# Kernel tuning notes

Hardware: AMD Instinct MI355X
Metric: run time of the kernel (lower is better)

Reference implementation:

```python
import jax, jax.numpy as jnp
import numpy as np
import math

NP2 = 64      # number of RF pulses
V = 32768     # number of voxels


def _shift_matrix(kmax):
    """EPG shift matrix, exact translation of EPG_shift_matrices."""
    N = 3 * (kmax + 1)
    S = np.zeros(N * N, dtype=np.complex64)
    kidx = list(range(3, N, 3)); sidx = [x - 3 for x in kidx]
    S[[a + N * b for a, b in zip(kidx, sidx)]] = 1
    kidx = list(range(4, N, 3)); kidx.pop(); sidx = [x + 3 for x in kidx]
    S[[a + N * b for a, b in zip(kidx, sidx)]] = 1
    kidx = list(range(2, N, 3))
    S[[a + N * b for a, b in zip(kidx, kidx)]] = 1
    S = S.reshape(N, N).T.copy()
    S[0:2, 4] = 1
    return jnp.asarray(S, dtype=jnp.complex64)


def _rf_rot_all(theta):
    """RF rotation matrices for all pulses at once. theta: [P] complex -> [P,3,3]."""
    a = jnp.abs(theta)
    phi = jnp.angle(theta)
    ca2 = (jnp.cos(a / 2) ** 2).astype(jnp.complex64)
    sa2 = jnp.sin(a / 2) ** 2
    sa = jnp.sin(a)
    ca = jnp.cos(a).astype(jnp.complex64)
    ep = jnp.exp(1j * phi)
    em = jnp.exp(-1j * phi)
    e2m = jnp.exp(-2j * phi)
    r00 = ca2
    r10 = e2m * sa2
    r20 = -0.5j * em * sa
    r01 = jnp.conj(r10)
    r11 = ca2
    r21 = 0.5j * ep * sa
    r02 = -1j * ep * sa
    r12 = 1j * em * sa
    r22 = ca
    row0 = jnp.stack([r00, r01, r02], axis=-1)
    row1 = jnp.stack([r10, r11, r12], axis=-1)
    row2 = jnp.stack([r20, r21, r22], axis=-1)
    return jnp.stack([row0, row1, row2], axis=-2).astype(jnp.complex64)


def _epg_gre_f0(theta, T1, T2, TR):
    """Single-compartment GRE EPG recurrence. Returns F0 signal [V, np2].

    Uses full-width (kmax) state updates every pulse: states beyond
    kmax_per_pulse are exactly zero on the ramp-up and cannot influence
    F0 on the ramp-down, so F0 matches the variable-width torch loop.
    """
    np2 = theta.shape[0]
    kmax = np2 - 1
    kpp_max = math.ceil(np2 / 2)
    if kpp_max < kmax:
        kmax = kpp_max
    K = kmax + 1
    N = 3 * K
    v = T1.shape[0]

    St = _shift_matrix(kmax).T                      # [N,N], so S @ f == f @ St
    E1 = jnp.exp(-TR / T1)[:, 0]                    # [V]
    E2 = jnp.exp(-TR / T2)[:, 0]                    # [V]
    # diagonal of kron(I_K, diag(E2,E2,E1)) per voxel -> [V,N]
    e = jnp.tile(jnp.stack([E2, E2, E1], axis=1), (1, K)).astype(jnp.complex64)
    b = jnp.zeros((v, N), jnp.complex64).at[:, 2].set((1 - E1).astype(jnp.complex64))

    A_all = _rf_rot_all(theta)                      # [np2,3,3]
    FF0 = jnp.zeros((v, N), jnp.complex64).at[:, 2].set(1.0)

    def step(FF, A):
        # block-diag kron(I_K, A) applied to the state vector
        Fcol = jnp.einsum('ab,vkb->vka', A, FF.reshape(v, K, 3)).reshape(v, N)
        # relaxation * shift + recovery
        FFn = e * (Fcol @ St) + b
        FFn = FFn.at[:, 0].set(jnp.conj(FFn[:, 0]))
        return FFn, Fcol[:, 0]

    _, F0 = jax.lax.scan(step, FF0, A_all)          # F0: [np2, V]
    return F0.T                                     # [V, np2]


def setup_inputs() -> dict:
    key = jax.random.key(0)
    k1, k2, k3, k4, k5 = jax.random.split(key, 5)
    flip = jax.random.uniform(k1, (NP2,), minval=0.1, maxval=math.pi / 2)
    phase = jax.random.uniform(k2, (NP2,), minval=-math.pi, maxval=math.pi)
    theta_re = (flip * jnp.cos(phase)).astype(jnp.float32)
    theta_im = (flip * jnp.sin(phase)).astype(jnp.float32)
    PD = jax.random.uniform(k3, (V, 1), minval=0.2, maxval=1.0)
    T1 = jax.random.uniform(k4, (V, 1), minval=300.0, maxval=1500.0)
    T2 = jax.random.uniform(k5, (V, 1), minval=20.0, maxval=120.0)
    qmaps = jnp.stack([PD, T1, T2], axis=0).astype(jnp.float32)  # [3,V,1]
    TR = jnp.array([10.0], jnp.float32)
    return {"theta_re": theta_re, "theta_im": theta_im, "TR": TR,
            "quantitative_maps": qmaps}


def reference(theta_re, theta_im, TR, quantitative_maps):
    theta = (theta_re + 1j * theta_im).astype(jnp.complex64)
    PD = quantitative_maps[0]   # [V,1]
    T1 = quantitative_maps[1]   # [V,1]
    T2 = quantitative_maps[2]   # [V,1]
    s = _epg_gre_f0(theta, T1, T2, TR)   # [V, np2] complex
    return jnp.abs(s) * PD
```

## Files before the change

### kernel.cpp

```cpp
#include <hip/hip_runtime.h>
#include <math.h>


#define NP2 64
#define ROR1  0x121
#define ROR15 0x12F

typedef float v2f __attribute__((ext_vector_type(2)));
typedef float v8f __attribute__((ext_vector_type(8)));

template<int CTRL>
__device__ __forceinline__ float rowrot(float x) {
    return __int_as_float(
        __builtin_amdgcn_mov_dpp(__float_as_int(x), CTRL, 0xF, 0xF, true));
}
__device__ __forceinline__ v2f mk2(float a, float b) { v2f r; r.x = a; r.y = b; return r; }

#define PAIR(V, i)  __builtin_shufflevector((V), (V), (i), (i) + 1)
#define FMA2(a, b, c) __builtin_elementwise_fma((a), (b), (c))

__global__ void coef_kernel(const float* __restrict__ theta_re,
                            const float* __restrict__ theta_im,
                            float* __restrict__ cw)
{
    const int t = threadIdx.x;
    if (t < NP2) {
        const float tre = theta_re[t], tim = theta_im[t];
        const float a2 = tre * tre + tim * tim;
        const float inva = __frsqrt_rn(a2);
        const float a = a2 * inva;
        const float c = tre * inva, s = tim * inva;
        float sa, ca;
        __sincosf(a, &sa, &ca);
        const float ca2 = 0.5f + 0.5f * ca;
        const float sa2 = 0.5f - 0.5f * ca;
        const float t1 = (c * c - s * s) * sa2;
        const float t2 = (2.f * c * s) * sa2;
        const float t3 = s * sa, t4 = c * sa;
        const float h3 = 0.5f * t3, h4 = 0.5f * t4;
        float4* row = (float4*)(cw + t * 24);
        row[0] = make_float4(ca2, ca2,  t1,  t1);
        row[1] = make_float4( t2,  t2, -t2, -t2);
        row[2] = make_float4( t3,  t3,  t4,  t4);
        row[3] = make_float4(-t4, -t4,  ca,  ca);
        row[4] = make_float4(-h3, -h3,  h4,  h4);
        row[5] = make_float4(-h4, -h4, 0.f, 0.f);
    } else if (t < NP2 + 6) {
        ((float4*)(cw + NP2 * 24))[t - NP2] = make_float4(0.f, 0.f, 0.f, 0.f);
    }
}

__global__ __launch_bounds__(256, 8) void epg_kernel(
    const float* __restrict__ TRp,
    const float* __restrict__ qmaps,
    const float* __restrict__ cw,
    float* __restrict__ out, int V)
{
    const int t = threadIdx.x;
    const int sub = t & 15;
    const int vloc = t >> 4;
    const int v = blockIdx.x * 16 + vloc;

    __shared__ __align__(16) v2f bufc[16][65];

    const float T1 = qmaps[V + v];
    const float T2 = qmaps[2 * V + v];
    const float tr = TRp[0];
    const float E1 = __expf(-tr / T1);
    const float E2 = __expf(-tr / T2);
    const v2f pE1 = mk2(E1, E1);
    const v2f pE2 = mk2(E2, E2);
    const float rE1s = (sub == 0) ? (1.0f - E1) : 0.0f;

    v2f Pr = mk2(0.f, 0.f), Pi = Pr, Mr = Pr, Mi = Pr, Zr = Pr, Zi = Pr;
    if (sub == 0) Zr.x = 1.0f;

    const bool s0 = (sub == 0);
    const bool s15 = (sub == 15);

    v8f A0, A1, A2, B0, B1, B2;
    asm volatile("s_load_dwordx8 %0, %1, 0x0"  : "=s"(B0) : "s"(cw));
    asm volatile("s_load_dwordx8 %0, %1, 0x20" : "=s"(B1) : "s"(cw));
    asm volatile("s_load_dwordx8 %0, %1, 0x40" : "=s"(B2) : "s"(cw));
    asm volatile("s_waitcnt lgkmcnt(0)"
                 : "=s"(A0), "=s"(A1), "=s"(A2) : "0"(B0), "1"(B1), "2"(B2));

#pragma unroll 1
    for (int p = 0; p < NP2; ++p) {
        const float* nx = cw + (p + 1) * 24;
        asm volatile("s_load_dwordx8 %0, %1, 0x0"  : "=s"(B0) : "s"(nx));
        asm volatile("s_load_dwordx8 %0, %1, 0x20" : "=s"(B1) : "s"(nx));
        asm volatile("s_load_dwordx8 %0, %1, 0x40" : "=s"(B2) : "s"(nx));

        const v2f Cca2 = PAIR(A0, 0), Ct1  = PAIR(A0, 2);
        const v2f Ct2  = PAIR(A0, 4), Cnt2 = PAIR(A0, 6);
        const v2f Ct3  = PAIR(A1, 0), Ct4  = PAIR(A1, 2);
        const v2f Cnt4 = PAIR(A1, 4), Cca  = PAIR(A1, 6);
        const v2f Cnh3 = PAIR(A2, 0), Ch4  = PAIR(A2, 2), Cnh4 = PAIR(A2, 4);

        const v2f nPr = FMA2(Cca2, Pr, FMA2(Ct1,  Mr, FMA2(Cnt2, Mi, FMA2(Ct3,  Zr, Ct4  * Zi))));
        const v2f nPi = FMA2(Cca2, Pi, FMA2(Ct2,  Mr, FMA2(Ct1,  Mi, FMA2(Cnt4, Zr, Ct3  * Zi))));
        const v2f nMr = FMA2(Ct1,  Pr, FMA2(Ct2,  Pi, FMA2(Cca2, Mr, FMA2(Ct3,  Zr, Cnt4 * Zi))));
        const v2f nMi = FMA2(Cnt2, Pr, FMA2(Ct1,  Pi, FMA2(Cca2, Mi, FMA2(Ct4,  Zr, Ct3  * Zi))));
        const v2f nZr = FMA2(Cnh3, Pr, FMA2(Ch4,  Pi, FMA2(Cnh3, Mr, FMA2(Cnh4, Mi, Cca  * Zr))));
        const v2f nZi = FMA2(Cnh4, Pr, FMA2(Cnh3, Pi, FMA2(Ch4,  Mr, FMA2(Cnh3, Mi, Cca  * Zi))));

        if (s0) bufc[vloc][p] = mk2(nPr.x, nPi.x);

        Pr = nPr * pE2; Pi = nPi * pE2;
        Mr = nMr * pE2; Mi = nMi * pE2;
        Zr = nZr * pE1; Zi = nZi * pE1;
        Zr.x += rE1s;

        const float rPrx = rowrot<ROR1>(Pr.x),  rPry = rowrot<ROR1>(Pr.y);
        const float rPix = rowrot<ROR1>(Pi.x),  rPiy = rowrot<ROR1>(Pi.y);
        const float rMrx = rowrot<ROR15>(Mr.x), rMry = rowrot<ROR15>(Mr.y);
        const float rMix = rowrot<ROR15>(Mi.x), rMiy = rowrot<ROR15>(Mi.y);
        Pr.y = s0 ?  rPrx : rPry;
        Pi.y = s0 ?  rPix : rPiy;
        Pr.x = s0 ?  rMrx : rPrx;
        Pi.x = s0 ? -rMix : rPix;
        Mr.x = s15 ? rMry : rMrx;
        Mi.x = s15 ? rMiy : rMix;
        Mr.y = s15 ? 0.f : rMry;
        Mi.y = s15 ? 0.f : rMiy;

        asm volatile("s_waitcnt lgkmcnt(0)"
                     : "=s"(A0), "=s"(A1), "=s"(A2) : "0"(B0), "1"(B1), "2"(B2));
    }

    __syncthreads();
    const int r = t >> 4;
    const int c = (t & 15) * 4;
    const float PDr = qmaps[blockIdx.x * 16 + r];
    const v2f a = bufc[r][c],     b = bufc[r][c + 1];
    const v2f d = bufc[r][c + 2], e = bufc[r][c + 3];
    float4 val;
    val.x = sqrtf(a.x * a.x + a.y * a.y) * PDr;
    val.y = sqrtf(b.x * b.x + b.y * b.y) * PDr;
    val.z = sqrtf(d.x * d.x + d.y * d.y) * PDr;
    val.w = sqrtf(e.x * e.x + e.y * e.y) * PDr;
    ((float4*)out)[blockIdx.x * 256 + t] = val;
}

extern "C" void kernel_launch(void* const* d_in, const int* in_sizes, int n_in,
                              void* d_out, int out_size, void* d_ws, size_t ws_size,
                              hipStream_t stream) {
    const float* theta_re = (const float*)d_in[0];
    const float* theta_im = (const float*)d_in[1];
    const float* TRp      = (const float*)d_in[2];
    const float* qmaps    = (const float*)d_in[3];
    float* out = (float*)d_out;
    float* cw  = (float*)d_ws;
    const int V = in_sizes[3] / 3;
    coef_kernel<<<dim3(1), dim3(128), 0, stream>>>(theta_re, theta_im, cw);
    epg_kernel<<<dim3(V / 16), dim3(256), 0, stream>>>(TRp, qmaps, cw, out, V);
}
```

Measured before the change: 115.3 us.

## Factor RF rotation into phase-difference rotation and real rotation with fused relaxation

Precomputes each pulse's phase relative to the previous pulse, so the per-pulse rotation becomes a complex phase rotation followed by a real-coefficient mixing. Relaxation is folded into the phase rotation coefficients, which shortens the per-step FMA chain and cuts the coefficient table from 24 to 16 floats per pulse. This relies on the phase-accumulation algebra being exact and may change rounding slightly.

```diff
diff --git a/kernel.cpp b/kernel.cpp
--- a/kernel.cpp
+++ b/kernel.cpp
@@ -30,23 +30,26 @@
         const float inva = __frsqrt_rn(a2);
         const float a = a2 * inva;
         const float c = tre * inva, s = tim * inva;
+        float cp = 1.f, sp = 0.f;
+        if (t > 0) {
+            const float ure = theta_re[t - 1], uim = theta_im[t - 1];
+            const float ia = __frsqrt_rn(ure * ure + uim * uim);
+            cp = ure * ia; sp = uim * ia;
+        }
+        const float cd = cp * c + sp * s;
+        const float sd = sp * c - cp * s;
         float sa, ca;
         __sincosf(a, &sa, &ca);
         const float ca2 = 0.5f + 0.5f * ca;
         const float sa2 = 0.5f - 0.5f * ca;
-        const float t1 = (c * c - s * s) * sa2;
-        const float t2 = (2.f * c * s) * sa2;
-        const float t3 = s * sa, t4 = c * sa;
-        const float h3 = 0.5f * t3, h4 = 0.5f * t4;
-        float4* row = (float4*)(cw + t * 24);
-        row[0] = make_float4(ca2, ca2,  t1,  t1);
-        row[1] = make_float4( t2,  t2, -t2, -t2);
-        row[2] = make_float4( t3,  t3,  t4,  t4);
-        row[3] = make_float4(-t4, -t4,  ca,  ca);
-        row[4] = make_float4(-h3, -h3,  h4,  h4);
-        row[5] = make_float4(-h4, -h4, 0.f, 0.f);
-    } else if (t < NP2 + 6) {
-        ((float4*)(cw + NP2 * 24))[t - NP2] = make_float4(0.f, 0.f, 0.f, 0.f);
+        const float h = 0.5f * sa;
+        float4* row = (float4*)(cw + t * 16);
+        row[0] = make_float4(cd, cd, sd, sd);
+        row[1] = make_float4(ca2, ca2, sa2, sa2);
+        row[2] = make_float4(sa, sa, ca, ca);
+        row[3] = make_float4(h, h, 0.f, 0.f);
+    } else if (t < NP2 + 4) {
+        ((float4*)(cw + NP2 * 16))[t - NP2] = make_float4(0.f, 0.f, 0.f, 0.f);
     }
 }
 
@@ -78,44 +81,48 @@
     const bool s0 = (sub == 0);
     const bool s15 = (sub == 15);
 
-    v8f A0, A1, A2, B0, B1, B2;
+    v8f A0, A1, B0, B1;
     asm volatile("s_load_dwordx8 %0, %1, 0x0"  : "=s"(B0) : "s"(cw));
     asm volatile("s_load_dwordx8 %0, %1, 0x20" : "=s"(B1) : "s"(cw));
-    asm volatile("s_load_dwordx8 %0, %1, 0x40" : "=s"(B2) : "s"(cw));
     asm volatile("s_waitcnt lgkmcnt(0)"
-                 : "=s"(A0), "=s"(A1), "=s"(A2) : "0"(B0), "1"(B1), "2"(B2));
+                 : "=s"(A0), "=s"(A1) : "0"(B0), "1"(B1));
 
 #pragma unroll 1
     for (int p = 0; p < NP2; ++p) {
-        const float* nx = cw + (p + 1) * 24;
+        const float* nx = cw + (p + 1) * 16;
         asm volatile("s_load_dwordx8 %0, %1, 0x0"  : "=s"(B0) : "s"(nx));
         asm volatile("s_load_dwordx8 %0, %1, 0x20" : "=s"(B1) : "s"(nx));
-        asm volatile("s_load_dwordx8 %0, %1, 0x40" : "=s"(B2) : "s"(nx));
 
-        const v2f Cca2 = PAIR(A0, 0), Ct1  = PAIR(A0, 2);
-        const v2f Ct2  = PAIR(A0, 4), Cnt2 = PAIR(A0, 6);
-        const v2f Ct3  = PAIR(A1, 0), Ct4  = PAIR(A1, 2);
-        const v2f Cnt4 = PAIR(A1, 4), Cca  = PAIR(A1, 6);
-        const v2f Cnh3 = PAIR(A2, 0), Ch4  = PAIR(A2, 2), Cnh4 = PAIR(A2, 4);
+        const v2f Ccd  = PAIR(A0, 0), Csd  = PAIR(A0, 2);
+        const v2f Cca2 = PAIR(A0, 4), Csa2 = PAIR(A0, 6);
+        const v2f Csa  = PAIR(A1, 0), Cca  = PAIR(A1, 2), Ch = PAIR(A1, 4);
 
-        const v2f nPr = FMA2(Cca2, Pr, FMA2(Ct1,  Mr, FMA2(Cnt2, Mi, FMA2(Ct3,  Zr, Ct4  * Zi))));
-        const v2f nPi = FMA2(Cca2, Pi, FMA2(Ct2,  Mr, FMA2(Ct1,  Mi, FMA2(Cnt4, Zr, Ct3  * Zi))));
-        const v2f nMr = FMA2(Ct1,  Pr, FMA2(Ct2,  Pi, FMA2(Cca2, Mr, FMA2(Ct3,  Zr, Cnt4 * Zi))));
-        const v2f nMi = FMA2(Cnt2, Pr, FMA2(Ct1,  Pi, FMA2(Cca2, Mi, FMA2(Ct4,  Zr, Ct3  * Zi))));
-        const v2f nZr = FMA2(Cnh3, Pr, FMA2(Ch4,  Pi, FMA2(Cnh3, Mr, FMA2(Cnh4, Mi, Cca  * Zr))));
-        const v2f nZi = FMA2(Cnh4, Pr, FMA2(Cnh3, Pi, FMA2(Ch4,  Mr, FMA2(Cnh3, Mi, Cca  * Zi))));
+        const v2f ec = pE2 * Ccd, es = pE2 * Csd;
+        const v2f hPr = FMA2(ec, Pr, -(es * Pi));
+        const v2f hPi = FMA2(ec, Pi,  (es * Pr));
+        const v2f hMr = FMA2(ec, Mr,  (es * Mi));
+        const v2f hMi = FMA2(ec, Mi, -(es * Mr));
+        v2f ezr = pE1 * Zr;
+        const v2f ezi = pE1 * Zi;
+        ezr.x += rE1s;
+
+        const v2f szr = Csa * ezr, szi = Csa * ezi;
+        const v2f nPr = FMA2(Cca2, hPr, FMA2(Csa2, hMr,  szi));
+        const v2f nPi = FMA2(Cca2, hPi, FMA2(Csa2, hMi, -szr));
+        const v2f nMr = FMA2(Csa2, hPr, FMA2(Cca2, hMr, -szi));
+        const v2f nMi = FMA2(Csa2, hPi, FMA2(Cca2, hMi,  szr));
+        const v2f d1 = hPi - hMi, d2 = hMr - hPr;
+        const v2f nZr = FMA2(Ch, d1, Cca * ezr);
+        const v2f nZi = FMA2(Ch, d2, Cca * ezi);
 
         if (s0) bufc[vloc][p] = mk2(nPr.x, nPi.x);
 
-        Pr = nPr * pE2; Pi = nPi * pE2;
-        Mr = nMr * pE2; Mi = nMi * pE2;
-        Zr = nZr * pE1; Zi = nZi * pE1;
-        Zr.x += rE1s;
+        Zr = nZr; Zi = nZi;
 
-        const float rPrx = rowrot<ROR1>(Pr.x),  rPry = rowrot<ROR1>(Pr.y);
-        const float rPix = rowrot<ROR1>(Pi.x),  rPiy = rowrot<ROR1>(Pi.y);
-        const float rMrx = rowrot<ROR15>(Mr.x), rMry = rowrot<ROR15>(Mr.y);
-        const float rMix = rowrot<ROR15>(Mi.x), rMiy = rowrot<ROR15>(Mi.y);
+        const float rPrx = rowrot<ROR1>(nPr.x),  rPry = rowrot<ROR1>(nPr.y);
+        const float rPix = rowrot<ROR1>(nPi.x),  rPiy = rowrot<ROR1>(nPi.y);
+        const float rMrx = rowrot<ROR15>(nMr.x), rMry = rowrot<ROR15>(nMr.y);
+        const float rMix = rowrot<ROR15>(nMi.x), rMiy = rowrot<ROR15>(nMi.y);
         Pr.y = s0 ?  rPrx : rPry;
         Pi.y = s0 ?  rPix : rPiy;
         Pr.x = s0 ?  rMrx : rPrx;
@@ -126,7 +133,7 @@
         Mi.y = s15 ? 0.f : rMiy;
 
         asm volatile("s_waitcnt lgkmcnt(0)"
-                     : "=s"(A0), "=s"(A1), "=s"(A2) : "0"(B0), "1"(B1), "2"(B2));
+                     : "=s"(A0), "=s"(A1) : "0"(B0), "1"(B1));
     }
 
     __syncthreads();
```

Result: faster. 109.0 us (-5.5%).
